# Optimization experiments

Hardware: AMD Instinct MI355X
Metric: run time of the kernel (lower is better)

## Reference

```python
import jax, jax.numpy as jnp
import numpy as np

DIMS = [64, 32, 12, 8, 6, 2]


def setup_inputs() -> dict:
    key = jax.random.key(0)
    ks = jax.random.split(key, 1 + 2 * (len(DIMS) - 1))
    inp = {"x": jax.random.normal(ks[0], (1048576, DIMS[0]), dtype=jnp.float32)}
    for i in range(len(DIMS) - 1):
        fan_in = DIMS[i]
        bound = 1.0 / np.sqrt(fan_in)
        inp[f"W{i}"] = jax.random.uniform(ks[1 + 2 * i], (DIMS[i], DIMS[i + 1]), jnp.float32, -bound, bound)
        inp[f"b{i}"] = jax.random.uniform(ks[2 + 2 * i], (DIMS[i + 1],), jnp.float32, -bound, bound)
    return inp


def reference(x, W0, b0, W1, b1, W2, b2, W3, b3, W4, b4):
    # 5-layer Linear+ReLU chain (final layer has no ReLU), matching nn.Sequential.
    h = jax.nn.relu(x @ W0 + b0)
    h = jax.nn.relu(h @ W1 + b1)
    h = jax.nn.relu(h @ W2 + b2)
    h = jax.nn.relu(h @ W3 + b3)
    return h @ W4 + b4  # [B, 2]
```

## Files before the change

kernel.cpp:

```cpp
#include <hip/hip_runtime.h>


typedef __attribute__((ext_vector_type(8))) short short8;
typedef __attribute__((ext_vector_type(16))) float f32x16;
typedef __attribute__((ext_vector_type(4))) unsigned uint4v;

#define BLOCK 256
#define NT 8

__device__ __forceinline__ unsigned fbits(float x) {
    return __builtin_bit_cast(unsigned, x);
}
__device__ __forceinline__ float asf(unsigned u) {
    return __builtin_bit_cast(float, u);
}
__device__ __forceinline__ unsigned packhi(unsigned ua, unsigned ub) {
    return __builtin_amdgcn_perm(ub, ua, 0x07060302u);
}
__device__ __forceinline__ short8 mk_hi(const float* f) {
    uint4v w;
#pragma unroll
    for (int t = 0; t < 4; ++t)
        w[t] = packhi(fbits(f[2 * t]), fbits(f[2 * t + 1]));
    return __builtin_bit_cast(short8, w);
}
__device__ __forceinline__ short8 mk_lo(const float* f) {
    uint4v w;
#pragma unroll
    for (int t = 0; t < 4; ++t) {
        const float la = f[2 * t]     - asf(fbits(f[2 * t])     & 0xFFFF0000u);
        const float lb = f[2 * t + 1] - asf(fbits(f[2 * t + 1]) & 0xFFFF0000u);
        w[t] = packhi(fbits(la), fbits(lb));
    }
    return __builtin_bit_cast(short8, w);
}
#define MFMA(A, B, C) __builtin_amdgcn_mfma_f32_32x32x16_bf16(A, B, C, 0, 0, 0)

template <int IN, int OUT, bool RELU>
__device__ __forceinline__ void layer(const float* __restrict__ W,
                                      const float* __restrict__ b,
                                      const float* h_in, float* h_out) {
#pragma unroll
    for (int o = 0; o < OUT; ++o) h_out[o] = b[o];
#pragma unroll
    for (int i = 0; i < IN; ++i) {
        const float v = h_in[i];
#pragma unroll
        for (int o = 0; o < OUT; ++o)
            h_out[o] = fmaf(v, W[i * OUT + o], h_out[o]);
    }
    if (RELU) {
#pragma unroll
        for (int o = 0; o < OUT; ++o) h_out[o] = fmaxf(h_out[o], 0.0f);
    }
}

__global__ __launch_bounds__(BLOCK, 2) void mlp_kernel(
        const float* __restrict__ x,
        const float* __restrict__ W0, const float* __restrict__ b0,
        const float* __restrict__ W1, const float* __restrict__ b1,
        const float* __restrict__ W2, const float* __restrict__ b2,
        const float* __restrict__ W3, const float* __restrict__ b3,
        const float* __restrict__ W4, const float* __restrict__ b4,
        float* __restrict__ out, int nrows) {
    const int t = threadIdx.x;
    const int wv = t >> 6;
    const int lane = t & 63;

    const long long row0 = ((long long)blockIdx.x * 4 + wv) * (NT * 64);
    const char* hbase = reinterpret_cast<const char*>(x + row0 * 64) +
                        (lane & 31) * 256 + (lane >> 5) * 32;

    const int hA = lane >> 5;
    const int colB = lane & 31;

    short8 W0h_, W0l_, W1h_, W1l_, W2h_, W2l_, W3h_, W3l_;
    {
        float wf[8];
#define LOADW(s, BH, BL)                                                \
        {                                                               \
            _Pragma("unroll")                                           \
            for (int j = 0; j < 8; ++j)                                 \
                wf[j] = W0[((s) * 16 + 8 * hA + j) * 32 + colB];        \
            BH = mk_hi(wf);                                             \
            BL = mk_lo(wf);                                             \
        }
        LOADW(0, W0h_, W0l_)
        LOADW(1, W1h_, W1l_)
        LOADW(2, W2h_, W2l_)
        LOADW(3, W3h_, W3l_)
#undef LOADW
    }

    float4 A0, A1, A2, A3, A4, A5, A6, A7;
    float4 B0, B1, B2, B3, B4, B5, B6, B7;

#define LOADH(OFF, P)                                                      \
    P##0 = *reinterpret_cast<const float4*>(hbase + (OFF) + 0);            \
    P##1 = *reinterpret_cast<const float4*>(hbase + (OFF) + 16);           \
    P##2 = *reinterpret_cast<const float4*>(hbase + (OFF) + 64);           \
    P##3 = *reinterpret_cast<const float4*>(hbase + (OFF) + 80);           \
    P##4 = *reinterpret_cast<const float4*>(hbase + (OFF) + 128);          \
    P##5 = *reinterpret_cast<const float4*>(hbase + (OFF) + 144);          \
    P##6 = *reinterpret_cast<const float4*>(hbase + (OFF) + 192);          \
    P##7 = *reinterpret_cast<const float4*>(hbase + (OFF) + 208);          \
    __builtin_amdgcn_sched_barrier(0);

#define KSTEP(Q0, Q1, WH, WL, ACC)                                         \
    {                                                                      \
        float f[8];                                                        \
        f[0] = Q0.x; f[1] = Q0.y; f[2] = Q0.z; f[3] = Q0.w;                \
        f[4] = Q1.x; f[5] = Q1.y; f[6] = Q1.z; f[7] = Q1.w;                \
        const short8 Xh = mk_hi(f), Xl = mk_lo(f);                         \
        ACC = MFMA(WH, Xh, ACC);                                           \
        ACC = MFMA(WL, Xh, ACC);                                           \
        ACC = MFMA(WH, Xl, ACC);                                           \
    }

    LOADH(0, A)

#pragma unroll 1
    for (int tt = 0; tt < NT; ++tt) {
        const long long toff = (long long)tt * 16384;

        f32x16 accA, accB;
#pragma unroll
        for (int r = 0; r < 16; ++r) { accA[r] = 0.0f; accB[r] = 0.0f; }

        LOADH(toff + 8192, B)
        KSTEP(A0, A1, W0h_, W0l_, accA)
        KSTEP(A2, A3, W1h_, W1l_, accA)
        KSTEP(A4, A5, W2h_, W2l_, accA)
        KSTEP(A6, A7, W3h_, W3l_, accA)

        if (tt + 1 < NT) {
            LOADH(toff + 16384, A)
        }
        KSTEP(B0, B1, W0h_, W0l_, accB)
        KSTEP(B2, B3, W1h_, W1l_, accB)
        KSTEP(B4, B5, W2h_, W2l_, accB)
        KSTEP(B6, B7, W3h_, W3l_, accB)

        float xr[32];
#pragma unroll
        for (int reg = 0; reg < 16; ++reg) {
            float a = accA[reg];
            float b = accB[reg];
            asm("v_permlane32_swap_b32 %0, %1" : "+v"(a), "+v"(b));
            const int f0 = (reg & 3) + 8 * (reg >> 2);
            xr[f0]     = fmaxf(a + b0[f0],     0.0f);
            xr[f0 + 4] = fmaxf(b + b0[f0 + 4], 0.0f);
        }

        float h1[12], h2[8], h3[6], h4[2];
        layer<32, 12, true>(W1, b1, xr, h1);
        layer<12, 8, true>(W2, b2, h1, h2);
        layer<8, 6, true>(W3, b3, h2, h3);
        layer<6, 2, false>(W4, b4, h3, h4);

        reinterpret_cast<float2*>(out)[row0 + tt * 64 + lane] =
            make_float2(h4[0], h4[1]);
    }
#undef LOADH
#undef KSTEP
}

extern "C" void kernel_launch(void* const* d_in, const int* in_sizes, int n_in,
                              void* d_out, int out_size, void* d_ws, size_t ws_size,
                              hipStream_t stream) {
    const float* x  = (const float*)d_in[0];
    const float* W0 = (const float*)d_in[1];
    const float* b0 = (const float*)d_in[2];
    const float* W1 = (const float*)d_in[3];
    const float* b1 = (const float*)d_in[4];
    const float* W2 = (const float*)d_in[5];
    const float* b2 = (const float*)d_in[6];
    const float* W3 = (const float*)d_in[7];
    const float* b3 = (const float*)d_in[8];
    const float* W4 = (const float*)d_in[9];
    const float* b4 = (const float*)d_in[10];
    float* out = (float*)d_out;

    const int nrows = in_sizes[0] / 64;
    const int rows_per_block = 4 * NT * 64;
    const int grid = nrows / rows_per_block;

    mlp_kernel<<<grid, BLOCK, 0, stream>>>(x, W0, b0, W1, b1, W2, b2,
                                           W3, b3, W4, b4, out, nrows);
}
```

Before: 55.91 us.

## Replace two-buffer input prefetch with rolling 4-slot load pipeline and raise occupancy

Replaces the double-buffered 16-float4 input staging with a rolling pipeline of four 2-float4 slots, issuing each chunk load about three MFMA k-steps ahead of its use. Register pressure drops, so launch bounds go from 2 to 4 waves-per-SIMD hint and rows per wave are halved (NT 8→4), doubling the grid. Layer-1 activations are read directly from the accumulators instead of being copied into an array. The aim is to hide HBM latency with finer-grained overlap and higher occupancy, at the cost of less prefetch depth per wave and more blocks to launch.

```diff
diff --git a/kernel.cpp b/kernel.cpp
--- a/kernel.cpp
+++ b/kernel.cpp
@@ -6,7 +6,7 @@
 typedef __attribute__((ext_vector_type(4))) unsigned uint4v;
 
 #define BLOCK 256
-#define NT 8
+#define NT 4
 
 __device__ __forceinline__ unsigned fbits(float x) {
     return __builtin_bit_cast(unsigned, x);
@@ -55,7 +55,7 @@
     }
 }
 
-__global__ __launch_bounds__(BLOCK, 2) void mlp_kernel(
+__global__ __launch_bounds__(BLOCK, 4) void mlp_kernel(
         const float* __restrict__ x,
         const float* __restrict__ W0, const float* __restrict__ b0,
         const float* __restrict__ W1, const float* __restrict__ b1,
@@ -92,68 +92,81 @@
 #undef LOADW
     }
 
-    float4 A0, A1, A2, A3, A4, A5, A6, A7;
-    float4 B0, B1, B2, B3, B4, B5, B6, B7;
-
-#define LOADH(OFF, P)                                                      \
-    P##0 = *reinterpret_cast<const float4*>(hbase + (OFF) + 0);            \
-    P##1 = *reinterpret_cast<const float4*>(hbase + (OFF) + 16);           \
-    P##2 = *reinterpret_cast<const float4*>(hbase + (OFF) + 64);           \
-    P##3 = *reinterpret_cast<const float4*>(hbase + (OFF) + 80);           \
-    P##4 = *reinterpret_cast<const float4*>(hbase + (OFF) + 128);          \
-    P##5 = *reinterpret_cast<const float4*>(hbase + (OFF) + 144);          \
-    P##6 = *reinterpret_cast<const float4*>(hbase + (OFF) + 192);          \
-    P##7 = *reinterpret_cast<const float4*>(hbase + (OFF) + 208);          \
-    __builtin_amdgcn_sched_barrier(0);
-
-#define KSTEP(Q0, Q1, WH, WL, ACC)                                         \
+    float4 S0a, S0b, S1a, S1b, S2a, S2b, S3a, S3b;
+
+#define ISS(CIDX, TB, Sa, Sb)                                              \
+    Sa = *reinterpret_cast<const float4*>(                                 \
+        hbase + (TB) + ((CIDX) >> 2) * 8192 + ((CIDX) & 3) * 64);          \
+    Sb = *reinterpret_cast<const float4*>(                                 \
+        hbase + (TB) + ((CIDX) >> 2) * 8192 + ((CIDX) & 3) * 64 + 16);
+
+#define SB __builtin_amdgcn_sched_barrier(0);
+
+#define KST(Sa, Sb, WH, WL, ACC)                                           \
     {                                                                      \
         float f[8];                                                        \
-        f[0] = Q0.x; f[1] = Q0.y; f[2] = Q0.z; f[3] = Q0.w;                \
-        f[4] = Q1.x; f[5] = Q1.y; f[6] = Q1.z; f[7] = Q1.w;                \
+        f[0] = Sa.x; f[1] = Sa.y; f[2] = Sa.z; f[3] = Sa.w;                \
+        f[4] = Sb.x; f[5] = Sb.y; f[6] = Sb.z; f[7] = Sb.w;                \
         const short8 Xh = mk_hi(f), Xl = mk_lo(f);                         \
         ACC = MFMA(WH, Xh, ACC);                                           \
         ACC = MFMA(WL, Xh, ACC);                                           \
         ACC = MFMA(WH, Xl, ACC);                                           \
     }
 
-    LOADH(0, A)
+    ISS(0, 0, S0a, S0b)
+    ISS(1, 0, S1a, S1b)
+    ISS(2, 0, S2a, S2b)
+    SB
 
 #pragma unroll 1
     for (int tt = 0; tt < NT; ++tt) {
         const long long toff = (long long)tt * 16384;
+        const long long noff = toff + 16384;
 
         f32x16 accA, accB;
 #pragma unroll
         for (int r = 0; r < 16; ++r) { accA[r] = 0.0f; accB[r] = 0.0f; }
 
-        LOADH(toff + 8192, B)
-        KSTEP(A0, A1, W0h_, W0l_, accA)
-        KSTEP(A2, A3, W1h_, W1l_, accA)
-        KSTEP(A4, A5, W2h_, W2l_, accA)
-        KSTEP(A6, A7, W3h_, W3l_, accA)
-
-        if (tt + 1 < NT) {
-            LOADH(toff + 16384, A)
-        }
-        KSTEP(B0, B1, W0h_, W0l_, accB)
-        KSTEP(B2, B3, W1h_, W1l_, accB)
-        KSTEP(B4, B5, W2h_, W2l_, accB)
-        KSTEP(B6, B7, W3h_, W3l_, accB)
-
-        float xr[32];
+        ISS(3, toff, S3a, S3b) SB KST(S0a, S0b, W0h_, W0l_, accA)
+        ISS(4, toff, S0a, S0b) SB KST(S1a, S1b, W1h_, W1l_, accA)
+        ISS(5, toff, S1a, S1b) SB KST(S2a, S2b, W2h_, W2l_, accA)
+        ISS(6, toff, S2a, S2b) SB KST(S3a, S3b, W3h_, W3l_, accA)
+        ISS(7, toff, S3a, S3b) SB KST(S0a, S0b, W0h_, W0l_, accB)
+        if (tt + 1 < NT) { ISS(0, noff, S0a, S0b) }
+        SB KST(S1a, S1b, W1h_, W1l_, accB)
+        if (tt + 1 < NT) { ISS(1, noff, S1a, S1b) }
+        SB KST(S2a, S2b, W2h_, W2l_, accB)
+        if (tt + 1 < NT) { ISS(2, noff, S2a, S2b) }
+        SB KST(S3a, S3b, W3h_, W3l_, accB)
+
 #pragma unroll
         for (int reg = 0; reg < 16; ++reg) {
             float a = accA[reg];
             float b = accB[reg];
             asm("v_permlane32_swap_b32 %0, %1" : "+v"(a), "+v"(b));
             const int f0 = (reg & 3) + 8 * (reg >> 2);
-            xr[f0]     = fmaxf(a + b0[f0],     0.0f);
-            xr[f0 + 4] = fmaxf(b + b0[f0 + 4], 0.0f);
+            accA[reg] = fmaxf(a + b0[f0],     0.0f);
+            accB[reg] = fmaxf(b + b0[f0 + 4], 0.0f);
         }
 
-        float h1[12], h2[8], h3[6], h4[2];
-        layer<32, 12, true>(W1, b1, xr, h1);
+#define H0(f) ((((f) >> 2) & 1) ? accB[((f) & 3) + 4 * ((f) >> 3)]          \
+                                : accA[((f) & 3) + 4 * ((f) >> 3)])
+
+        float h1[12];
+#pragma unroll
+        for (int o = 0; o < 12; ++o) h1[o] = b1[o];
+#pragma unroll
+        for (int i = 0; i < 32; ++i) {
+            const float v = H0(i);
+#pragma unroll
+            for (int o = 0; o < 12; ++o)
+                h1[o] = fmaf(v, W1[i * 12 + o], h1[o]);
+        }
+#pragma unroll
+        for (int o = 0; o < 12; ++o) h1[o] = fmaxf(h1[o], 0.0f);
+#undef H0
+
+        float h2[8], h3[6], h4[2];
         layer<12, 8, true>(W2, b2, h1, h2);
         layer<8, 6, true>(W3, b3, h2, h3);
         layer<6, 2, false>(W4, b4, h3, h4);
@@ -161,8 +174,9 @@
         reinterpret_cast<float2*>(out)[row0 + tt * 64 + lane] =
             make_float2(h4[0], h4[1]);
     }
-#undef LOADH
-#undef KSTEP
+#undef ISS
+#undef KST
+#undef SB
 }
 
 extern "C" void kernel_launch(void* const* d_in, const int* in_sizes, int n_in,
```

Result: slower. 60.77 us (+8.7%).

## Stage input tiles through padded LDS with coalesced global loads

Applied to the files above, without the earlier changes.

Global loads of x become fully coalesced (each lane reads consecutive 16B chunks across 1KB rows) and are written into a padded, per-wave double-buffered LDS region. MFMA operands are then read from LDS with a padded row stride to avoid bank conflicts. The block size drops to 128 threads (two waves) so the grid doubles. This is meant to cut the strided, poorly coalesced global access pattern, at the cost of extra LDS traffic and LDS capacity limiting occupancy. No barriers are needed because each wave writes and reads only its own LDS buffer.

```diff
diff --git a/kernel.cpp b/kernel.cpp
--- a/kernel.cpp
+++ b/kernel.cpp
@@ -5,8 +5,10 @@
 typedef __attribute__((ext_vector_type(16))) float f32x16;
 typedef __attribute__((ext_vector_type(4))) unsigned uint4v;
 
-#define BLOCK 256
+#define BLOCK 128
 #define NT 8
+#define RSTRIDE 272
+#define HBYTES 8704
 
 __device__ __forceinline__ unsigned fbits(float x) {
     return __builtin_bit_cast(unsigned, x);
@@ -63,16 +65,21 @@
         const float* __restrict__ W3, const float* __restrict__ b3,
         const float* __restrict__ W4, const float* __restrict__ b4,
         float* __restrict__ out, int nrows) {
+    extern __shared__ char lds[];
     const int t = threadIdx.x;
     const int wv = t >> 6;
     const int lane = t & 63;
-
-    const long long row0 = ((long long)blockIdx.x * 4 + wv) * (NT * 64);
-    const char* hbase = reinterpret_cast<const char*>(x + row0 * 64) +
-                        (lane & 31) * 256 + (lane >> 5) * 32;
+    char* const buf0 = lds + wv * (2 * HBYTES);
+    char* const buf1 = buf0 + HBYTES;
+
+    const long long row0 = ((long long)blockIdx.x * 2 + wv) * (NT * 64);
+    const char* xbase = reinterpret_cast<const char*>(x + row0 * 64);
 
     const int hA = lane >> 5;
     const int colB = lane & 31;
+
+    const int wbase = (lane >> 4) * RSTRIDE + (lane & 15) * 16;
+    const int rb = (lane & 31) * RSTRIDE + hA * 32;
 
     short8 W0h_, W0l_, W1h_, W1l_, W2h_, W2l_, W3h_, W3l_;
     {
@@ -92,54 +99,74 @@
 #undef LOADW
     }
 
-    float4 A0, A1, A2, A3, A4, A5, A6, A7;
-    float4 B0, B1, B2, B3, B4, B5, B6, B7;
-
-#define LOADH(OFF, P)                                                      \
-    P##0 = *reinterpret_cast<const float4*>(hbase + (OFF) + 0);            \
-    P##1 = *reinterpret_cast<const float4*>(hbase + (OFF) + 16);           \
-    P##2 = *reinterpret_cast<const float4*>(hbase + (OFF) + 64);           \
-    P##3 = *reinterpret_cast<const float4*>(hbase + (OFF) + 80);           \
-    P##4 = *reinterpret_cast<const float4*>(hbase + (OFF) + 128);          \
-    P##5 = *reinterpret_cast<const float4*>(hbase + (OFF) + 144);          \
-    P##6 = *reinterpret_cast<const float4*>(hbase + (OFF) + 192);          \
-    P##7 = *reinterpret_cast<const float4*>(hbase + (OFF) + 208);          \
-    __builtin_amdgcn_sched_barrier(0);
-
-#define KSTEP(Q0, Q1, WH, WL, ACC)                                         \
+    float4 P0_0, P0_1, P0_2, P0_3, P0_4, P0_5, P0_6, P0_7;
+    float4 P1_0, P1_1, P1_2, P1_3, P1_4, P1_5, P1_6, P1_7;
+
+#define SB __builtin_amdgcn_sched_barrier(0);
+
+#define LOADD(h, P)                                                        \
+    {                                                                      \
+        const char* s0 = xbase + (long long)(h) * 8192 + lane * 16;        \
+        P##_0 = *reinterpret_cast<const float4*>(s0 + 0 * 1024);           \
+        P##_1 = *reinterpret_cast<const float4*>(s0 + 1 * 1024);           \
+        P##_2 = *reinterpret_cast<const float4*>(s0 + 2 * 1024);           \
+        P##_3 = *reinterpret_cast<const float4*>(s0 + 3 * 1024);           \
+        P##_4 = *reinterpret_cast<const float4*>(s0 + 4 * 1024);           \
+        P##_5 = *reinterpret_cast<const float4*>(s0 + 5 * 1024);           \
+        P##_6 = *reinterpret_cast<const float4*>(s0 + 6 * 1024);           \
+        P##_7 = *reinterpret_cast<const float4*>(s0 + 7 * 1024);           \
+    }                                                                      \
+    SB
+
+#define WLDS(P, BUF)                                                       \
+    *reinterpret_cast<float4*>((BUF) + wbase + 0 * 1088) = P##_0;          \
+    *reinterpret_cast<float4*>((BUF) + wbase + 1 * 1088) = P##_1;          \
+    *reinterpret_cast<float4*>((BUF) + wbase + 2 * 1088) = P##_2;          \
+    *reinterpret_cast<float4*>((BUF) + wbase + 3 * 1088) = P##_3;          \
+    *reinterpret_cast<float4*>((BUF) + wbase + 4 * 1088) = P##_4;          \
+    *reinterpret_cast<float4*>((BUF) + wbase + 5 * 1088) = P##_5;          \
+    *reinterpret_cast<float4*>((BUF) + wbase + 6 * 1088) = P##_6;          \
+    *reinterpret_cast<float4*>((BUF) + wbase + 7 * 1088) = P##_7;          \
+    SB
+
+#define KST(BUF, s, WH, WL, ACC)                                           \
     {                                                                      \
         float f[8];                                                        \
-        f[0] = Q0.x; f[1] = Q0.y; f[2] = Q0.z; f[3] = Q0.w;                \
-        f[4] = Q1.x; f[5] = Q1.y; f[6] = Q1.z; f[7] = Q1.w;                \
+        const float4 q0 =                                                  \
+            *reinterpret_cast<const float4*>((BUF) + rb + (s) * 64);       \
+        const float4 q1 =                                                  \
+            *reinterpret_cast<const float4*>((BUF) + rb + (s) * 64 + 16);  \
+        f[0] = q0.x; f[1] = q0.y; f[2] = q0.z; f[3] = q0.w;                \
+        f[4] = q1.x; f[5] = q1.y; f[6] = q1.z; f[7] = q1.w;                \
         const short8 Xh = mk_hi(f), Xl = mk_lo(f);                         \
         ACC = MFMA(WH, Xh, ACC);                                           \
         ACC = MFMA(WL, Xh, ACC);                                           \
         ACC = MFMA(WH, Xl, ACC);                                           \
     }
 
-    LOADH(0, A)
+    LOADD(0, P0)
+    LOADD(1, P1)
+    WLDS(P0, buf0)
 
 #pragma unroll 1
     for (int tt = 0; tt < NT; ++tt) {
-        const long long toff = (long long)tt * 16384;
-
         f32x16 accA, accB;
 #pragma unroll
         for (int r = 0; r < 16; ++r) { accA[r] = 0.0f; accB[r] = 0.0f; }
 
-        LOADH(toff + 8192, B)
-        KSTEP(A0, A1, W0h_, W0l_, accA)
-        KSTEP(A2, A3, W1h_, W1l_, accA)
-        KSTEP(A4, A5, W2h_, W2l_, accA)
-        KSTEP(A6, A7, W3h_, W3l_, accA)
-
-        if (tt + 1 < NT) {
-            LOADH(toff + 16384, A)
-        }
-        KSTEP(B0, B1, W0h_, W0l_, accB)
-        KSTEP(B2, B3, W1h_, W1l_, accB)
-        KSTEP(B4, B5, W2h_, W2l_, accB)
-        KSTEP(B6, B7, W3h_, W3l_, accB)
+        if (2 * tt + 2 < 2 * NT) { LOADD(2 * tt + 2, P0) }
+        WLDS(P1, buf1)
+        KST(buf0, 0, W0h_, W0l_, accA)
+        KST(buf0, 1, W1h_, W1l_, accA)
+        KST(buf0, 2, W2h_, W2l_, accA)
+        KST(buf0, 3, W3h_, W3l_, accA)
+
+        if (2 * tt + 3 < 2 * NT) { LOADD(2 * tt + 3, P1) }
+        if (2 * tt + 2 < 2 * NT) { WLDS(P0, buf0) }
+        KST(buf1, 0, W0h_, W0l_, accB)
+        KST(buf1, 1, W1h_, W1l_, accB)
+        KST(buf1, 2, W2h_, W2l_, accB)
+        KST(buf1, 3, W3h_, W3l_, accB)
 
         float xr[32];
 #pragma unroll
@@ -161,8 +188,10 @@
         reinterpret_cast<float2*>(out)[row0 + tt * 64 + lane] =
             make_float2(h4[0], h4[1]);
     }
-#undef LOADH
-#undef KSTEP
+#undef LOADD
+#undef WLDS
+#undef KST
+#undef SB
 }
 
 extern "C" void kernel_launch(void* const* d_in, const int* in_sizes, int n_in,
@@ -182,9 +211,10 @@
     float* out = (float*)d_out;
 
     const int nrows = in_sizes[0] / 64;
-    const int rows_per_block = 4 * NT * 64;
+    const int rows_per_block = 2 * NT * 64;
     const int grid = nrows / rows_per_block;
-
-    mlp_kernel<<<grid, BLOCK, 0, stream>>>(x, W0, b0, W1, b1, W2, b2,
-                                           W3, b3, W4, b4, out, nrows);
-}
+    const size_t shmem = 2 * 2 * HBYTES;
+
+    mlp_kernel<<<grid, BLOCK, shmem, stream>>>(x, W0, b0, W1, b1, W2, b2,
+                                               W3, b3, W4, b4, out, nrows);
+}
```

Result: no change. 55.70 us (-0.4%).
